# Kernel tuning notes

Hardware: AMD Instinct MI355X
Metric: run time of the kernel (lower is better)

The kernel has to match this reference:

```python
import jax, jax.numpy as jnp
import numpy as np

NUM_HEADS = 12


def setup_inputs() -> dict:
    key = jax.random.key(0)
    ks = jax.random.split(key, 5)
    B, N, C = 64, 388, 768  # N = 8*8*2 + 16*16 + 4
    return {
        "x": jax.random.normal(ks[0], (B, N, C), dtype=jnp.float32),
        "qkv_w": jax.random.normal(ks[1], (3 * C, C), dtype=jnp.float32) * 0.02,
        "qkv_b": jax.random.normal(ks[2], (3 * C,), dtype=jnp.float32) * 0.02,
        "proj_w": jax.random.normal(ks[3], (C, C), dtype=jnp.float32) * 0.02,
        "proj_b": jax.random.normal(ks[4], (C,), dtype=jnp.float32) * 0.02,
        "t_h": 8, "t_w": 8, "s_h": 16, "s_w": 16,
    }


def reference(x, qkv_w, qkv_b, proj_w, proj_b, t_h, t_w, s_h, s_w):
    B, N, C = x.shape
    H = NUM_HEADS
    D = C // H
    scale = D ** -0.5
    L_t = t_h * t_w * 2          # template (x2) tokens
    L_s = s_h * s_w + 4          # search tokens + 4 extra

    qkv = x @ qkv_w.T + qkv_b                       # [B,N,3C]
    qkv = qkv.reshape(B, N, 3, H, D).transpose(2, 0, 3, 1, 4)  # [3,B,H,N,D]
    q, k, v = qkv[0], qkv[1], qkv[2]                # each [B,H,N,D]

    q_mt, q_s = q[:, :, :L_t], q[:, :, L_t:]
    k_mt = k[:, :, :L_t]
    v_mt = v[:, :, :L_t]

    # template self-attention (template queries attend only to template keys)
    attn_mt = jax.nn.softmax(jnp.einsum("bhqd,bhkd->bhqk", q_mt, k_mt) * scale, axis=-1)
    x_mt = jnp.einsum("bhqk,bhkd->bhqd", attn_mt, v_mt)  # [B,H,L_t,D]
    x_mt = x_mt.transpose(0, 2, 1, 3).reshape(B, L_t, C)

    # search queries attend to ALL keys
    attn_s = jax.nn.softmax(jnp.einsum("bhqd,bhkd->bhqk", q_s, k) * scale, axis=-1)
    x_s = jnp.einsum("bhqk,bhkd->bhqd", attn_s, v)  # [B,H,L_s,D]
    x_s = x_s.transpose(0, 2, 1, 3).reshape(B, L_s, C)

    out = jnp.concatenate([x_mt, x_s], axis=1)      # [B,N,C]
    out = out @ proj_w.T + proj_b
    return out
```

## Files before the change

### kernel.cpp

```cpp
#include <hip/hip_runtime.h>
#include <cstdint>
#include <cstddef>
#include <cmath>

typedef __attribute__((ext_vector_type(4))) float f32x4;
typedef __attribute__((ext_vector_type(8))) short bf16x8;

typedef const __attribute__((address_space(1))) void* gas_ptr;
typedef __attribute__((address_space(3))) void* las_ptr;

static __device__ __forceinline__ short f2bf(float f) {
    union { float f; uint32_t u; } v; v.f = f;
    uint32_t r = v.u + 0x7fffu + ((v.u >> 16) & 1u);
    return (short)(r >> 16);
}

constexpr int MP = 25088;

__global__ void cvt_f32_bf16(const float* __restrict__ src, short* __restrict__ dst, int n4) {
    int i = blockIdx.x * blockDim.x + threadIdx.x;
    const int stride = gridDim.x * blockDim.x;
    for (; i < n4; i += stride) {
        const float4 v = reinterpret_cast<const float4*>(src)[i];
        short4 o;
        o.x = f2bf(v.x); o.y = f2bf(v.y); o.z = f2bf(v.z); o.w = f2bf(v.w);
        reinterpret_cast<short4*>(dst)[i] = o;
    }
}

__global__ void cvt_x_pad(const float* __restrict__ src, short* __restrict__ dst) {
    constexpr int N4 = MP * 768 / 4;
    int i = blockIdx.x * blockDim.x + threadIdx.x;
    const int stride = gridDim.x * blockDim.x;
    for (; i < N4; i += stride) {
        const int flat = i * 4;
        const int mp  = flat / 768;
        const int col = flat - mp * 768;
        const int b   = mp / 392;
        const int nn  = mp - b * 392;
        short4 o;
        if (nn < 388) {
            const float4 v = *reinterpret_cast<const float4*>(
                src + ((size_t)(b * 388 + nn) * 768 + col));
            o.x = f2bf(v.x); o.y = f2bf(v.y); o.z = f2bf(v.z); o.w = f2bf(v.w);
        } else {
            o.x = 0; o.y = 0; o.z = 0; o.w = 0;
        }
        reinterpret_cast<short4*>(dst)[i] = o;
    }
}

template<int MODE>
__global__ __launch_bounds__(256) void gemm_bt(
    const short* __restrict__ A, const short* __restrict__ Bw,
    const float* __restrict__ bias,
    short* __restrict__ qk, short* __restrict__ vT,
    float* __restrict__ fo, int NB)
{
    constexpr int K = 768;
    constexpr int KT = 12;
    __shared__ __align__(16) short ldsraw[2 * 128 * 64 * 2];
    short* ldsA = ldsraw;
    short* ldsB = ldsraw + 2 * 128 * 64;

    const int tid  = threadIdx.x;
    const int lane = tid & 63;
    const int wid  = tid >> 6;
    const int lrow = lane & 15;
    const int lgrp = lane >> 4;
    const int wr   = wid >> 1;
    const int wc   = wid & 1;

    const int nwg = gridDim.x;
    const int q8  = nwg >> 3, r8 = nwg & 7;
    const int xcd = blockIdx.x & 7, bidx = blockIdx.x >> 3;
    const int wgid = (xcd < r8 ? xcd * (q8 + 1) : r8 * (q8 + 1) + (xcd - r8) * q8) + bidx;

    int m0, n0;
    if constexpr (MODE == 0) {
        constexpr int G = 14, SG = G * 18;
        const int mg = wgid / SG;
        const int r  = wgid - mg * SG;
        const int n  = r / G;
        const int mi = r - n * G;
        m0 = (mg * G + mi) * 128;
        n0 = n * 128;
    } else {
        m0 = (wgid / NB) * 128;
        n0 = (wgid % NB) * 128;
    }

    f32x4 acc[4][4];
    #pragma unroll
    for (int i = 0; i < 4; ++i)
        #pragma unroll
        for (int j = 0; j < 4; ++j)
            acc[i][j] = f32x4{0.f, 0.f, 0.f, 0.f};

    auto stage = [&](int kt, int buf) {
        #pragma unroll
        for (int it = 0; it < 4; ++it) {
            const int c   = it * 256 + wid * 64 + lane;
            const int row = c >> 3;
            const int scb = ((c & 7) * 16) ^ ((row & 7) << 4);
            const short* ga = A  + (size_t)(m0 + row) * K + kt * 64 + (scb >> 1);
            const short* gb = Bw + (size_t)(n0 + row) * K + kt * 64 + (scb >> 1);
            __builtin_amdgcn_global_load_lds((gas_ptr)ga, (las_ptr)((char*)(ldsA + buf * 128 * 64) + c * 16), 16, 0, 0);
            __builtin_amdgcn_global_load_lds((gas_ptr)gb, (las_ptr)((char*)(ldsB + buf * 128 * 64) + c * 16), 16, 0, 0);
        }
    };

    stage(0, 0);

    for (int kt = 0; kt < KT; ++kt) {
        const int cur = kt & 1;
        if (kt + 1 < KT) {
            stage(kt + 1, cur ^ 1);
            asm volatile("s_waitcnt vmcnt(8)" ::: "memory");
        } else {
            asm volatile("s_waitcnt vmcnt(0)" ::: "memory");
        }
        __builtin_amdgcn_s_barrier();
        __builtin_amdgcn_sched_barrier(0);

        #pragma unroll
        for (int ks = 0; ks < 2; ++ks) {
            bf16x8 af[4], bfv[4];
            #pragma unroll
            for (int i = 0; i < 4; ++i) {
                const int r   = wr * 64 + i * 16 + lrow;
                const int byt = r * 128 + ((ks * 64 + lgrp * 16) ^ ((r & 7) << 4));
                af[i] = *reinterpret_cast<const bf16x8*>((const char*)(ldsA + cur * 128 * 64) + byt);
            }
            #pragma unroll
            for (int j = 0; j < 4; ++j) {
                const int r   = wc * 64 + j * 16 + lrow;
                const int byt = r * 128 + ((ks * 64 + lgrp * 16) ^ ((r & 7) << 4));
                bfv[j] = *reinterpret_cast<const bf16x8*>((const char*)(ldsB + cur * 128 * 64) + byt);
            }
            #pragma unroll
            for (int i = 0; i < 4; ++i)
                #pragma unroll
                for (int j = 0; j < 4; ++j)
                    acc[i][j] = __builtin_amdgcn_mfma_f32_16x16x32_bf16(af[i], bfv[j], acc[i][j], 0, 0, 0);
        }

        __builtin_amdgcn_sched_barrier(0);
        __builtin_amdgcn_s_barrier();
    }

    const int mb = m0 + wr * 64;
    const int nb = n0 + wc * 64;
    if constexpr (MODE == 0) {
        if (n0 < 1536) {
            #pragma unroll
            for (int j = 0; j < 4; ++j) {
                const int c  = nb + j * 16 + lrow;
                const float sc = (c < 768) ? 0.18033688011116f : 1.0f;
                const float bv = bias[c];
                #pragma unroll
                for (int i = 0; i < 4; ++i) {
                    #pragma unroll
                    for (int r = 0; r < 4; ++r) {
                        const int m = mb + i * 16 + lgrp * 4 + r;
                        qk[(size_t)m * 1536 + c] = f2bf((acc[i][j][r] + bv) * sc);
                    }
                }
            }
        } else {
            const int h = (nb - 1536) >> 6;
            short* lw = ldsraw + wid * (64 * 80);
            #pragma unroll
            for (int j = 0; j < 4; ++j) {
                const int dloc = j * 16 + lrow;
                const float bv = bias[nb + j * 16 + lrow];
                #pragma unroll
                for (int i = 0; i < 4; ++i)
                    #pragma unroll
                    for (int r = 0; r < 4; ++r)
                        lw[dloc * 80 + i * 16 + lgrp * 4 + r] = f2bf(acc[i][j][r] + bv);
            }
            asm volatile("s_waitcnt lgkmcnt(0)" ::: "memory");
            __builtin_amdgcn_sched_barrier(0);
            #pragma unroll
            for (int w = 0; w < 8; ++w) {
                const int d    = w * 8 + (lane >> 3);
                const int nloc = (lane & 7) * 8;
                const bf16x8 val = *reinterpret_cast<const bf16x8*>(lw + d * 80 + nloc);
                const int mchunk = mb + nloc;
                const int b  = mchunk / 392;
                const int nn = mchunk - b * 392;
                short* dst = vT + ((size_t)(b * 12 + h) * 64 + d) * 392 + nn;
                *reinterpret_cast<bf16x8*>(dst) = val;
            }
        }
    } else {
        #pragma unroll
        for (int i = 0; i < 4; ++i) {
            #pragma unroll
            for (int r = 0; r < 4; ++r) {
                const int m = mb + i * 16 + lgrp * 4 + r;
                #pragma unroll
                for (int j = 0; j < 4; ++j) {
                    const int c = nb + j * 16 + lrow;
                    fo[(size_t)m * 768 + c] = acc[i][j][r] + bias[c];
                }
            }
        }
    }
}

constexpr int PSTRB = 256;

template<int NT, bool VLDS>
static __device__ __forceinline__ void attn_chunk_lds(
    int kbeg, int k_len,
    const short* __restrict__ klds, const short* __restrict__ vlds,
    const short* __restrict__ vglob,
    const bf16x8 (&qf)[2], char* __restrict__ my,
    int lrow, int lgrp,
    float (&rs)[4], f32x4 (&oacc)[4])
{
    f32x4 sacc[NT];
    #pragma unroll
    for (int t = 0; t < NT; ++t) sacc[t] = f32x4{0.f, 0.f, 0.f, 0.f};

    #pragma unroll
    for (int t = 0; t < NT; ++t) {
        const int kl   = t * 16 + lrow;
        const int byt0 = kl * 128 + ((lgrp * 16) ^ ((kl & 7) << 4));
        const int byt1 = kl * 128 + ((64 + lgrp * 16) ^ ((kl & 7) << 4));
        const bf16x8 k0 = *reinterpret_cast<const bf16x8*>((const char*)klds + byt0);
        const bf16x8 k1 = *reinterpret_cast<const bf16x8*>((const char*)klds + byt1);
        sacc[t] = __builtin_amdgcn_mfma_f32_16x16x32_bf16(qf[0], k0, sacc[t], 0, 0, 0);
        sacc[t] = __builtin_amdgcn_mfma_f32_16x16x32_bf16(qf[1], k1, sacc[t], 0, 0, 0);
    }
    #pragma unroll
    for (int t = 0; t < NT; ++t) {
        const bool bad = (kbeg + t * 16 + lrow >= k_len);
        #pragma unroll
        for (int r = 0; r < 4; ++r) {
            const float p = bad ? 0.f : exp2f(sacc[t][r]);
            rs[r] += p;
            const int row = lgrp * 4 + r;
            const int byt = row * PSTRB + ((t * 32 + lrow * 2) ^ ((row & 7) << 4));
            *reinterpret_cast<short*>(my + byt) = f2bf(p);
        }
    }

    #pragma unroll
    for (int ks = 0; ks < NT / 2; ++ks) {
        const bf16x8 pf = *reinterpret_cast<const bf16x8*>(
            my + lrow * PSTRB + ((ks * 64 + lgrp * 16) ^ ((lrow & 7) << 4)));
        #pragma unroll
        for (int dt = 0; dt < 4; ++dt) {
            const int d = dt * 16 + lrow;
            const bf16x8 vf = VLDS
                ? *reinterpret_cast<const bf16x8*>((const char*)vlds + d * 256 + ((ks * 64 + lgrp * 16) ^ ((d & 7) << 4)))
                : *reinterpret_cast<const bf16x8*>(vglob + (size_t)d * 392 + ks * 32 + lgrp * 8);
            oacc[dt] = __builtin_amdgcn_mfma_f32_16x16x32_bf16(pf, vf, oacc[dt], 0, 0, 0);
        }
    }
}

__global__ __launch_bounds__(256, 2) void attn_flash(
    const short* __restrict__ qkb, const short* __restrict__ vT,
    short* __restrict__ ao)
{
    __shared__ __align__(16) short klds[2][128 * 64];
    __shared__ __align__(16) short vlds[2][64 * 128];
    __shared__ __align__(16) char  plds[4][16 * PSTRB];

    const int tid  = threadIdx.x;
    const int lane = tid & 63;
    const int wid  = tid >> 6;
    const int lrow = lane & 15;
    const int lgrp = lane >> 4;

    const int blk = blockIdx.x;
    const int xcd = blk & 7;
    const int i7  = blk >> 3;
    const int bh  = xcd * 96 + i7 / 7;
    const int bx  = i7 % 7;

    int q_start, qend, k_len, nfull;
    bool tail;
    if (bx < 2) { q_start = bx * 64;             qend = 128; k_len = 128; nfull = 1; tail = false; }
    else        { q_start = 128 + (bx - 2) * 64; qend = 388; k_len = 388; nfull = 3; tail = true;  }

    const int q0 = q_start + wid * 16;

    const int b = bh / 12, h = bh - b * 12;
    const short* qbase = qkb + (size_t)b * 392 * 1536 + h * 64;
    const short* kbase = qbase + 768;
    const short* vbase = vT + (size_t)bh * 64 * 392;

    int qrow = q0 + lrow; if (qrow >= qend) qrow = qend - 1;
    bf16x8 qf[2];
    #pragma unroll
    for (int ks = 0; ks < 2; ++ks)
        qf[ks] = *reinterpret_cast<const bf16x8*>(qbase + (size_t)qrow * 1536 + ks * 32 + lgrp * 8);

    float rs[4] = {0.f, 0.f, 0.f, 0.f};
    f32x4 oacc[4];
    #pragma unroll
    for (int dt = 0; dt < 4; ++dt) oacc[dt] = f32x4{0.f, 0.f, 0.f, 0.f};

    char* my = &plds[wid][0];

    auto stage_full = [&](int ch, int buf) {
        const int kbeg = ch * 128;
        #pragma unroll
        for (int it = 0; it < 4; ++it) {
            const int c = it * 256 + tid;
            const int krow = c >> 3;
            const int kscb = ((c & 7) * 16) ^ ((krow & 7) << 4);
            const short* gk = kbase + (size_t)(kbeg + krow) * 1536 + (kscb >> 1);
            __builtin_amdgcn_global_load_lds((gas_ptr)gk, (las_ptr)((char*)&klds[buf][0] + c * 16), 16, 0, 0);
            const int vrow = c >> 4;
            const int vscb = ((c & 15) * 16) ^ ((vrow & 7) << 4);
            const short* gv = vbase + (size_t)vrow * 392 + kbeg + (vscb >> 1);
            __builtin_amdgcn_global_load_lds((gas_ptr)gv, (las_ptr)((char*)&vlds[buf][0] + c * 16), 16, 0, 0);
        }
    };

    stage_full(0, 0);

    for (int ch = 0; ch < nfull; ++ch) {
        const int cur = ch & 1;
        if (ch + 1 < nfull) {
            stage_full(ch + 1, cur ^ 1);
            asm volatile("s_waitcnt vmcnt(8)" ::: "memory");
        } else {
            asm volatile("s_waitcnt vmcnt(0)" ::: "memory");
        }
        __builtin_amdgcn_s_barrier();
        __builtin_amdgcn_sched_barrier(0);

        attn_chunk_lds<8, true>(ch * 128, k_len, &klds[cur][0], &vlds[cur][0],
                                nullptr, qf, my, lrow, lgrp, rs, oacc);

        __builtin_amdgcn_sched_barrier(0);
        __builtin_amdgcn_s_barrier();
    }

    if (tail) {
        {
            const int c = tid;
            const int krow = c >> 3;
            const int kscb = ((c & 7) * 16) ^ ((krow & 7) << 4);
            int g = 384 + krow; if (g > 391) g = 391;
            const short* gk = kbase + (size_t)g * 1536 + (kscb >> 1);
            __builtin_amdgcn_global_load_lds((gas_ptr)gk, (las_ptr)((char*)&klds[0][0] + c * 16), 16, 0, 0);
        }
        asm volatile("s_waitcnt vmcnt(0)" ::: "memory");
        __builtin_amdgcn_s_barrier();
        __builtin_amdgcn_sched_barrier(0);

        attn_chunk_lds<2, false>(384, k_len, &klds[0][0], nullptr, vbase + 384,
                                 qf, my, lrow, lgrp, rs, oacc);
    }

    #pragma unroll
    for (int msk = 1; msk < 16; msk <<= 1)
        #pragma unroll
        for (int r = 0; r < 4; ++r) rs[r] += __shfl_xor(rs[r], msk, 64);

    float inv[4];
    #pragma unroll
    for (int r = 0; r < 4; ++r) inv[r] = 1.0f / rs[r];
    #pragma unroll
    for (int r = 0; r < 4; ++r) {
        const int qn = q0 + lgrp * 4 + r;
        if (qn < qend) {
            #pragma unroll
            for (int dt = 0; dt < 4; ++dt)
                ao[((size_t)b * 388 + qn) * 768 + h * 64 + dt * 16 + lrow] =
                    f2bf(oacc[dt][r] * inv[r]);
        }
    }
}

extern "C" void kernel_launch(void* const* d_in, const int* in_sizes, int n_in,
                              void* d_out, int out_size, void* d_ws, size_t ws_size,
                              hipStream_t stream) {
    (void)in_sizes; (void)n_in; (void)out_size; (void)ws_size;
    const float* x      = (const float*)d_in[0];
    const float* qkv_w  = (const float*)d_in[1];
    const float* qkv_b  = (const float*)d_in[2];
    const float* proj_w = (const float*)d_in[3];
    const float* proj_b = (const float*)d_in[4];
    float* out = (float*)d_out;

    char* ws = (char*)d_ws;
    short* xb   = (short*)(ws);
    short* attn = (short*)(ws);
    short* qkb  = (short*)(ws + 38535168);
    short* vTb  = (short*)(ws + 115605504);
    short* qwb  = (short*)(ws + 154140672);
    short* pwb  = (short*)(ws + 157679616);

    cvt_x_pad  <<<2048, 256, 0, stream>>>(x, xb);
    cvt_f32_bf16<<<512,  256, 0, stream>>>(qkv_w,  qwb, 2304 * 768 / 4);
    cvt_f32_bf16<<<256,  256, 0, stream>>>(proj_w, pwb, 768 * 768 / 4);

    gemm_bt<0><<<dim3(196 * 18), 256, 0, stream>>>(xb, qwb, qkv_b, qkb, vTb, nullptr, 18);

    attn_flash<<<dim3(5376), 256, 0, stream>>>(qkb, vTb, attn);

    gemm_bt<1><<<dim3(194 * 6), 256, 0, stream>>>(attn, pwb, proj_b, nullptr, nullptr, out, 6);
}
```

Measured before the change: 242.5 us.

## Use 256x256-tile 8-wave phased pipeline for the QKV GEMM

Replaces the templated 128x128 QKV GEMM with a dedicated kernel. It uses 256x256 output tiles, 512 threads (8 waves, each owning 128x64) and a double-buffered 128KB LDS. Each k-step is split into four phases that interleave LDS fragment reads, half-tile async global-to-LDS prefetches and MFMA batches raised with s_setprio. The aim is more operand reuse per loaded byte and better overlap of loads with matrix math. In exchange there are many more barriers, heavy register pressure from 32 accumulators, and only one workgroup per CU because of the LDS footprint. The projection GEMM is split out into its own non-templated kernel with unchanged behavior.

```diff
diff --git a/kernel.cpp b/kernel.cpp
--- a/kernel.cpp
+++ b/kernel.cpp
@@ -50,12 +50,217 @@
     }
 }
 
-template<int MODE>
-__global__ __launch_bounds__(256) void gemm_bt(
+__global__ __launch_bounds__(512, 2) void gemm_qkv_8ph(
     const short* __restrict__ A, const short* __restrict__ Bw,
     const float* __restrict__ bias,
-    short* __restrict__ qk, short* __restrict__ vT,
-    float* __restrict__ fo, int NB)
+    short* __restrict__ qk, short* __restrict__ vT)
+{
+    constexpr int K = 768;
+    constexpr int KT = 12;
+    __shared__ __align__(16) short lds[2][2][256 * 64];
+
+    const int tid  = threadIdx.x;
+    const int lane = tid & 63;
+    const int wid  = tid >> 6;
+    const int lrow = lane & 15;
+    const int lgrp = lane >> 4;
+    const int wr   = wid >> 2;
+    const int wc   = wid & 3;
+
+    const int nwg = gridDim.x;
+    const int q8  = nwg >> 3, r8 = nwg & 7;
+    const int xcd = blockIdx.x & 7, bidx = blockIdx.x >> 3;
+    const int wgid = (xcd < r8 ? xcd * (q8 + 1) : r8 * (q8 + 1) + (xcd - r8) * q8) + bidx;
+    constexpr int G = 14, SG = G * 9;
+    const int mg  = wgid / SG;
+    const int rr_ = wgid - mg * SG;
+    const int nn_ = rr_ / G;
+    const int mi  = rr_ - nn_ * G;
+    const int m0  = (mg * G + mi) * 256;
+    const int n0  = nn_ * 256;
+
+    f32x4 acc[8][4];
+    #pragma unroll
+    for (int i = 0; i < 8; ++i)
+        #pragma unroll
+        for (int j = 0; j < 4; ++j)
+            acc[i][j] = f32x4{0.f, 0.f, 0.f, 0.f};
+
+    auto stage_half = [&](int kt, int buf, int op, int half) {
+        const short* srcp = (op == 0) ? A : Bw;
+        const int rb = (op == 0) ? m0 : n0;
+        #pragma unroll
+        for (int it = 0; it < 2; ++it) {
+            const int c   = half * 1024 + it * 512 + tid;
+            const int row = c >> 3;
+            const int scb = ((c & 7) * 16) ^ ((row & 7) << 4);
+            const short* g = srcp + (size_t)(rb + row) * K + kt * 64 + (scb >> 1);
+            __builtin_amdgcn_global_load_lds((gas_ptr)g,
+                (las_ptr)((char*)&lds[buf][op][0] + c * 16), 16, 0, 0);
+        }
+    };
+
+    auto rdA = [&](int buf, int i, int ks) -> bf16x8 {
+        const int r   = wr * 128 + i * 16 + lrow;
+        const int byt = r * 128 + ((ks * 64 + lgrp * 16) ^ ((r & 7) << 4));
+        return *reinterpret_cast<const bf16x8*>((const char*)&lds[buf][0][0] + byt);
+    };
+    auto rdB = [&](int buf, int j, int ks) -> bf16x8 {
+        const int r   = wc * 64 + j * 16 + lrow;
+        const int byt = r * 128 + ((ks * 64 + lgrp * 16) ^ ((r & 7) << 4));
+        return *reinterpret_cast<const bf16x8*>((const char*)&lds[buf][1][0] + byt);
+    };
+
+    stage_half(0, 0, 0, 0); stage_half(0, 0, 0, 1);
+    stage_half(0, 0, 1, 0); stage_half(0, 0, 1, 1);
+    asm volatile("s_waitcnt vmcnt(0)" ::: "memory");
+    __builtin_amdgcn_s_barrier();
+
+    for (int t = 0; t < KT; ++t) {
+        const int cur = t & 1;
+        const int nxt = cur ^ 1;
+        const bool more = (t + 1 < KT);
+        bf16x8 a03[2][4], a47[2][4], b01[2][2], b23[2][2];
+
+        #pragma unroll
+        for (int ks = 0; ks < 2; ++ks) {
+            #pragma unroll
+            for (int i = 0; i < 4; ++i) a03[ks][i] = rdA(cur, i, ks);
+            #pragma unroll
+            for (int j = 0; j < 2; ++j) b01[ks][j] = rdB(cur, j, ks);
+        }
+        if (more) stage_half(t + 1, nxt, 0, 0);
+        __builtin_amdgcn_s_barrier();
+        asm volatile("s_waitcnt lgkmcnt(0)" ::: "memory");
+        __builtin_amdgcn_sched_barrier(0);
+        __builtin_amdgcn_s_setprio(1);
+        #pragma unroll
+        for (int ks = 0; ks < 2; ++ks)
+            #pragma unroll
+            for (int i = 0; i < 4; ++i)
+                #pragma unroll
+                for (int j = 0; j < 2; ++j)
+                    acc[i][j] = __builtin_amdgcn_mfma_f32_16x16x32_bf16(a03[ks][i], b01[ks][j], acc[i][j], 0, 0, 0);
+        __builtin_amdgcn_s_setprio(0);
+        __builtin_amdgcn_s_barrier();
+
+        #pragma unroll
+        for (int ks = 0; ks < 2; ++ks)
+            #pragma unroll
+            for (int j = 0; j < 2; ++j) b23[ks][j] = rdB(cur, 2 + j, ks);
+        if (more) stage_half(t + 1, nxt, 0, 1);
+        __builtin_amdgcn_s_barrier();
+        asm volatile("s_waitcnt lgkmcnt(0)" ::: "memory");
+        __builtin_amdgcn_sched_barrier(0);
+        __builtin_amdgcn_s_setprio(1);
+        #pragma unroll
+        for (int ks = 0; ks < 2; ++ks)
+            #pragma unroll
+            for (int i = 0; i < 4; ++i)
+                #pragma unroll
+                for (int j = 0; j < 2; ++j)
+                    acc[i][2 + j] = __builtin_amdgcn_mfma_f32_16x16x32_bf16(a03[ks][i], b23[ks][j], acc[i][2 + j], 0, 0, 0);
+        __builtin_amdgcn_s_setprio(0);
+        __builtin_amdgcn_s_barrier();
+
+        #pragma unroll
+        for (int ks = 0; ks < 2; ++ks)
+            #pragma unroll
+            for (int i = 0; i < 4; ++i) a47[ks][i] = rdA(cur, 4 + i, ks);
+        if (more) stage_half(t + 1, nxt, 1, 0);
+        __builtin_amdgcn_s_barrier();
+        asm volatile("s_waitcnt lgkmcnt(0)" ::: "memory");
+        __builtin_amdgcn_sched_barrier(0);
+        __builtin_amdgcn_s_setprio(1);
+        #pragma unroll
+        for (int ks = 0; ks < 2; ++ks)
+            #pragma unroll
+            for (int i = 0; i < 4; ++i)
+                #pragma unroll
+                for (int j = 0; j < 2; ++j)
+                    acc[4 + i][2 + j] = __builtin_amdgcn_mfma_f32_16x16x32_bf16(a47[ks][i], b23[ks][j], acc[4 + i][2 + j], 0, 0, 0);
+        __builtin_amdgcn_s_setprio(0);
+        __builtin_amdgcn_s_barrier();
+
+        #pragma unroll
+        for (int ks = 0; ks < 2; ++ks)
+            #pragma unroll
+            for (int j = 0; j < 2; ++j) b01[ks][j] = rdB(cur, j, ks);
+        if (more) stage_half(t + 1, nxt, 1, 1);
+        __builtin_amdgcn_s_barrier();
+        asm volatile("s_waitcnt lgkmcnt(0)" ::: "memory");
+        __builtin_amdgcn_sched_barrier(0);
+        __builtin_amdgcn_s_setprio(1);
+        #pragma unroll
+        for (int ks = 0; ks < 2; ++ks)
+            #pragma unroll
+            for (int i = 0; i < 4; ++i)
+                #pragma unroll
+                for (int j = 0; j < 2; ++j)
+                    acc[4 + i][j] = __builtin_amdgcn_mfma_f32_16x16x32_bf16(a47[ks][i], b01[ks][j], acc[4 + i][j], 0, 0, 0);
+        __builtin_amdgcn_s_setprio(0);
+
+        __builtin_amdgcn_sched_barrier(0);
+        asm volatile("s_waitcnt vmcnt(0)" ::: "memory");
+        __builtin_amdgcn_s_barrier();
+    }
+
+    const int mb = m0 + wr * 128;
+    const int nb = n0 + wc * 64;
+    if (n0 < 1536) {
+        #pragma unroll
+        for (int j = 0; j < 4; ++j) {
+            const int c  = nb + j * 16 + lrow;
+            const float sc = (c < 768) ? 0.18033688011116f : 1.0f;
+            const float bv = bias[c];
+            #pragma unroll
+            for (int i = 0; i < 8; ++i) {
+                #pragma unroll
+                for (int r = 0; r < 4; ++r) {
+                    const int m = mb + i * 16 + lgrp * 4 + r;
+                    qk[(size_t)m * 1536 + c] = f2bf((acc[i][j][r] + bv) * sc);
+                }
+            }
+        }
+    } else {
+        const int h = (nb - 1536) >> 6;
+        short* lw = (short*)&lds[0][0][0] + wid * (64 * 80);
+        #pragma unroll
+        for (int pass = 0; pass < 2; ++pass) {
+            if (pass) {
+                asm volatile("s_waitcnt lgkmcnt(0)" ::: "memory");
+                __builtin_amdgcn_sched_barrier(0);
+            }
+            #pragma unroll
+            for (int j = 0; j < 4; ++j) {
+                const int dloc = j * 16 + lrow;
+                const float bv = bias[nb + j * 16 + lrow];
+                #pragma unroll
+                for (int ii = 0; ii < 4; ++ii)
+                    #pragma unroll
+                    for (int r = 0; r < 4; ++r)
+                        lw[dloc * 80 + ii * 16 + lgrp * 4 + r] = f2bf(acc[pass * 4 + ii][j][r] + bv);
+            }
+            asm volatile("s_waitcnt lgkmcnt(0)" ::: "memory");
+            __builtin_amdgcn_sched_barrier(0);
+            #pragma unroll
+            for (int w = 0; w < 8; ++w) {
+                const int d    = w * 8 + (lane >> 3);
+                const int nloc = (lane & 7) * 8;
+                const bf16x8 val = *reinterpret_cast<const bf16x8*>(lw + d * 80 + nloc);
+                const int mchunk = mb + pass * 64 + nloc;
+                const int b  = mchunk / 392;
+                const int nn = mchunk - b * 392;
+                short* dst = vT + ((size_t)(b * 12 + h) * 64 + d) * 392 + nn;
+                *reinterpret_cast<bf16x8*>(dst) = val;
+            }
+        }
+    }
+}
+
+__global__ __launch_bounds__(256) void gemm_proj(
+    const short* __restrict__ A, const short* __restrict__ Bw,
+    const float* __restrict__ bias, float* __restrict__ fo, int NB)
 {
     constexpr int K = 768;
     constexpr int KT = 12;
@@ -75,20 +280,8 @@
     const int q8  = nwg >> 3, r8 = nwg & 7;
     const int xcd = blockIdx.x & 7, bidx = blockIdx.x >> 3;
     const int wgid = (xcd < r8 ? xcd * (q8 + 1) : r8 * (q8 + 1) + (xcd - r8) * q8) + bidx;
-
-    int m0, n0;
-    if constexpr (MODE == 0) {
-        constexpr int G = 14, SG = G * 18;
-        const int mg = wgid / SG;
-        const int r  = wgid - mg * SG;
-        const int n  = r / G;
-        const int mi = r - n * G;
-        m0 = (mg * G + mi) * 128;
-        n0 = n * 128;
-    } else {
-        m0 = (wgid / NB) * 128;
-        n0 = (wgid % NB) * 128;
-    }
+    const int m0 = (wgid / NB) * 128;
+    const int n0 = (wgid % NB) * 128;
 
     f32x4 acc[4][4];
     #pragma unroll
@@ -151,60 +344,15 @@
 
     const int mb = m0 + wr * 64;
     const int nb = n0 + wc * 64;
-    if constexpr (MODE == 0) {
-        if (n0 < 1536) {
+    #pragma unroll
+    for (int i = 0; i < 4; ++i) {
+        #pragma unroll
+        for (int r = 0; r < 4; ++r) {
+            const int m = mb + i * 16 + lgrp * 4 + r;
             #pragma unroll
             for (int j = 0; j < 4; ++j) {
-                const int c  = nb + j * 16 + lrow;
-                const float sc = (c < 768) ? 0.18033688011116f : 1.0f;
-                const float bv = bias[c];
-                #pragma unroll
-                for (int i = 0; i < 4; ++i) {
-                    #pragma unroll
-                    for (int r = 0; r < 4; ++r) {
-                        const int m = mb + i * 16 + lgrp * 4 + r;
-                        qk[(size_t)m * 1536 + c] = f2bf((acc[i][j][r] + bv) * sc);
-                    }
-                }
-            }
-        } else {
-            const int h = (nb - 1536) >> 6;
-            short* lw = ldsraw + wid * (64 * 80);
-            #pragma unroll
-            for (int j = 0; j < 4; ++j) {
-                const int dloc = j * 16 + lrow;
-                const float bv = bias[nb + j * 16 + lrow];
-                #pragma unroll
-                for (int i = 0; i < 4; ++i)
-                    #pragma unroll
-                    for (int r = 0; r < 4; ++r)
-                        lw[dloc * 80 + i * 16 + lgrp * 4 + r] = f2bf(acc[i][j][r] + bv);
-            }
-            asm volatile("s_waitcnt lgkmcnt(0)" ::: "memory");
-            __builtin_amdgcn_sched_barrier(0);
-            #pragma unroll
-            for (int w = 0; w < 8; ++w) {
-                const int d    = w * 8 + (lane >> 3);
-                const int nloc = (lane & 7) * 8;
-                const bf16x8 val = *reinterpret_cast<const bf16x8*>(lw + d * 80 + nloc);
-                const int mchunk = mb + nloc;
-                const int b  = mchunk / 392;
-                const int nn = mchunk - b * 392;
-                short* dst = vT + ((size_t)(b * 12 + h) * 64 + d) * 392 + nn;
-                *reinterpret_cast<bf16x8*>(dst) = val;
-            }
-        }
-    } else {
-        #pragma unroll
-        for (int i = 0; i < 4; ++i) {
-            #pragma unroll
-            for (int r = 0; r < 4; ++r) {
-                const int m = mb + i * 16 + lgrp * 4 + r;
-                #pragma unroll
-                for (int j = 0; j < 4; ++j) {
-                    const int c = nb + j * 16 + lrow;
-                    fo[(size_t)m * 768 + c] = acc[i][j][r] + bias[c];
-                }
+                const int c = nb + j * 16 + lrow;
+                fo[(size_t)m * 768 + c] = acc[i][j][r] + bias[c];
             }
         }
     }
@@ -404,9 +552,9 @@
     cvt_f32_bf16<<<512,  256, 0, stream>>>(qkv_w,  qwb, 2304 * 768 / 4);
     cvt_f32_bf16<<<256,  256, 0, stream>>>(proj_w, pwb, 768 * 768 / 4);
 
-    gemm_bt<0><<<dim3(196 * 18), 256, 0, stream>>>(xb, qwb, qkv_b, qkb, vTb, nullptr, 18);
+    gemm_qkv_8ph<<<dim3(98 * 9), 512, 0, stream>>>(xb, qwb, qkv_b, qkb, vTb);
 
     attn_flash<<<dim3(5376), 256, 0, stream>>>(qkb, vTb, attn);
 
-    gemm_bt<1><<<dim3(194 * 6), 256, 0, stream>>>(attn, pwb, proj_b, nullptr, nullptr, out, 6);
-}
+    gemm_proj<<<dim3(194 * 6), 256, 0, stream>>>(attn, pwb, proj_b, out, 6);
+}
```

Result: slower. 272.1 us (+12.2%).

## Replace 128x128 GEMM with 256x256 eight-wave tile and phased prefetch schedule

Applied to the files above, without the earlier changes.

The QKV and projection GEMMs now use 256x256 output tiles with 512 threads, 8 waves and a 128 KB double-buffered LDS. This replaces the 128x128 tiles with 4 waves. The K loop is split into phases that interleave quarter-tile global-to-LDS prefetches with MFMA blocks, using barriers and s_setprio to overlap loads with compute and raise operand reuse. The V-transpose epilogue runs in two passes to fit the larger accumulator. In exchange, fewer and larger workgroups raise register pressure, allow only one block per CU, and may give worse wave-quantization tails.

```diff
diff --git a/kernel.cpp b/kernel.cpp
--- a/kernel.cpp
+++ b/kernel.cpp
@@ -50,26 +50,45 @@
     }
 }
 
+#define PH_SYNC() \
+    __builtin_amdgcn_s_barrier(); \
+    asm volatile("s_waitcnt lgkmcnt(0)" ::: "memory"); \
+    __builtin_amdgcn_sched_barrier(0); \
+    __builtin_amdgcn_s_setprio(1)
+
+#define PH_END() \
+    __builtin_amdgcn_s_setprio(0); \
+    __builtin_amdgcn_s_barrier()
+
+#define MFMA4x2(IOFF, JOFF, B) \
+    _Pragma("unroll") \
+    for (int ks = 0; ks < 2; ++ks) \
+        _Pragma("unroll") \
+        for (int i = 0; i < 4; ++i) \
+            _Pragma("unroll") \
+            for (int j = 0; j < 2; ++j) \
+                acc[(IOFF)+i][(JOFF)+j] = __builtin_amdgcn_mfma_f32_16x16x32_bf16( \
+                    a[ks][i], B[ks][j], acc[(IOFF)+i][(JOFF)+j], 0, 0, 0)
+
 template<int MODE>
-__global__ __launch_bounds__(256) void gemm_bt(
+__global__ __launch_bounds__(512, 2) void gemm256(
     const short* __restrict__ A, const short* __restrict__ Bw,
     const float* __restrict__ bias,
     short* __restrict__ qk, short* __restrict__ vT,
-    float* __restrict__ fo, int NB)
+    float* __restrict__ fo)
 {
     constexpr int K = 768;
     constexpr int KT = 12;
-    __shared__ __align__(16) short ldsraw[2 * 128 * 64 * 2];
-    short* ldsA = ldsraw;
-    short* ldsB = ldsraw + 2 * 128 * 64;
+    constexpr int NU = 6;
+    __shared__ __align__(16) short lds[2][2][256 * 64];
 
     const int tid  = threadIdx.x;
     const int lane = tid & 63;
     const int wid  = tid >> 6;
     const int lrow = lane & 15;
     const int lgrp = lane >> 4;
-    const int wr   = wid >> 1;
-    const int wc   = wid & 1;
+    const int wr   = wid >> 2;
+    const int wc   = wid & 3;
 
     const int nwg = gridDim.x;
     const int q8  = nwg >> 3, r8 = nwg & 7;
@@ -78,78 +97,144 @@
 
     int m0, n0;
     if constexpr (MODE == 0) {
-        constexpr int G = 14, SG = G * 18;
-        const int mg = wgid / SG;
-        const int r  = wgid - mg * SG;
-        const int n  = r / G;
-        const int mi = r - n * G;
-        m0 = (mg * G + mi) * 128;
-        n0 = n * 128;
+        constexpr int G = 14, SG = G * 9;
+        const int mg  = wgid / SG;
+        const int r_  = wgid - mg * SG;
+        const int nn_ = r_ / G;
+        m0 = (mg * G + (r_ - nn_ * G)) * 256;
+        n0 = nn_ * 256;
     } else {
-        m0 = (wgid / NB) * 128;
-        n0 = (wgid % NB) * 128;
-    }
-
-    f32x4 acc[4][4];
-    #pragma unroll
-    for (int i = 0; i < 4; ++i)
+        m0 = (wgid / 3) * 256;
+        n0 = (wgid % 3) * 256;
+    }
+
+    f32x4 acc[8][4];
+    #pragma unroll
+    for (int i = 0; i < 8; ++i)
         #pragma unroll
         for (int j = 0; j < 4; ++j)
             acc[i][j] = f32x4{0.f, 0.f, 0.f, 0.f};
 
-    auto stage = [&](int kt, int buf) {
-        #pragma unroll
-        for (int it = 0; it < 4; ++it) {
-            const int c   = it * 256 + wid * 64 + lane;
+    auto stage_piece = [&](int kt, int buf, int piece) {
+        const int op = (piece == 0 || piece == 3) ? 0 : 1;
+        const short* srcp = op ? Bw : A;
+        const int rb = op ? n0 : m0;
+        #pragma unroll
+        for (int it = 0; it < 2; ++it) {
+            int c;
+            if (piece == 0)      c = it * 1024 + tid;
+            else if (piece == 3) c = it * 1024 + 512 + tid;
+            else {
+                const int idx = it * 512 + tid;
+                const int grp = idx >> 8, win = idx & 255;
+                c = grp * 512 + ((piece == 2) ? 256 : 0) + win;
+            }
             const int row = c >> 3;
             const int scb = ((c & 7) * 16) ^ ((row & 7) << 4);
-            const short* ga = A  + (size_t)(m0 + row) * K + kt * 64 + (scb >> 1);
-            const short* gb = Bw + (size_t)(n0 + row) * K + kt * 64 + (scb >> 1);
-            __builtin_amdgcn_global_load_lds((gas_ptr)ga, (las_ptr)((char*)(ldsA + buf * 128 * 64) + c * 16), 16, 0, 0);
-            __builtin_amdgcn_global_load_lds((gas_ptr)gb, (las_ptr)((char*)(ldsB + buf * 128 * 64) + c * 16), 16, 0, 0);
+            const short* g = srcp + (size_t)(rb + row) * K + kt * 64 + (scb >> 1);
+            __builtin_amdgcn_global_load_lds((gas_ptr)g,
+                (las_ptr)((char*)&lds[buf][op][0] + c * 16), 16, 0, 0);
         }
     };
 
-    stage(0, 0);
-
-    for (int kt = 0; kt < KT; ++kt) {
-        const int cur = kt & 1;
-        if (kt + 1 < KT) {
-            stage(kt + 1, cur ^ 1);
-            asm volatile("s_waitcnt vmcnt(8)" ::: "memory");
-        } else {
-            asm volatile("s_waitcnt vmcnt(0)" ::: "memory");
-        }
+    auto rdA = [&](int buf, int i, int ks) -> bf16x8 {
+        const int r   = wr * 128 + i * 16 + lrow;
+        const int byt = r * 128 + ((ks * 64 + lgrp * 16) ^ ((r & 7) << 4));
+        return *reinterpret_cast<const bf16x8*>((const char*)&lds[buf][0][0] + byt);
+    };
+    auto rdB = [&](int buf, int j, int ks) -> bf16x8 {
+        const int r   = wc * 64 + j * 16 + lrow;
+        const int byt = r * 128 + ((ks * 64 + lgrp * 16) ^ ((r & 7) << 4));
+        return *reinterpret_cast<const bf16x8*>((const char*)&lds[buf][1][0] + byt);
+    };
+
+    stage_piece(0, 0, 0); stage_piece(0, 0, 1); stage_piece(0, 0, 2); stage_piece(0, 0, 3);
+    stage_piece(1, 1, 0); stage_piece(1, 1, 2);
+    asm volatile("s_waitcnt vmcnt(0)" ::: "memory");
+    __builtin_amdgcn_s_barrier();
+
+    bf16x8 a[2][4], bf0[2][2], bf1[2][2];
+
+    for (int u = 0; u < NU; ++u) {
+        const int t1  = 2 * u + 1;
+        const int tn0 = 2 * u + 2;
+        const int tn1 = 2 * u + 3;
+        const bool lastu = (u + 1 == NU);
+
+        #pragma unroll
+        for (int ks = 0; ks < 2; ++ks) {
+            #pragma unroll
+            for (int i = 0; i < 4; ++i) a[ks][i] = rdA(0, i, ks);
+            #pragma unroll
+            for (int j = 0; j < 2; ++j) bf0[ks][j] = rdB(0, j, ks);
+        }
+        stage_piece(t1, 1, 3);
+        PH_SYNC(); MFMA4x2(0, 0, bf0); PH_END();
+
+        #pragma unroll
+        for (int ks = 0; ks < 2; ++ks)
+            #pragma unroll
+            for (int j = 0; j < 2; ++j) bf1[ks][j] = rdB(0, 2 + j, ks);
+        stage_piece(t1, 1, 1);
+        PH_SYNC(); MFMA4x2(0, 2, bf1); PH_END();
+
+        #pragma unroll
+        for (int ks = 0; ks < 2; ++ks)
+            #pragma unroll
+            for (int i = 0; i < 4; ++i) a[ks][i] = rdA(0, 4 + i, ks);
+        if (tn0 < KT) stage_piece(tn0, 0, 0);
+        PH_SYNC(); MFMA4x2(4, 2, bf1); PH_END();
+
+        #pragma unroll
+        for (int ks = 0; ks < 2; ++ks)
+            #pragma unroll
+            for (int j = 0; j < 2; ++j) bf0[ks][j] = rdB(0, j, ks);
+        if (tn0 < KT) stage_piece(tn0, 0, 2);
+        PH_SYNC(); MFMA4x2(4, 0, bf0);
+        __builtin_amdgcn_s_setprio(0);
+        __builtin_amdgcn_sched_barrier(0);
+        if (!lastu) asm volatile("s_waitcnt vmcnt(4)" ::: "memory");
+        else        asm volatile("s_waitcnt vmcnt(0)" ::: "memory");
         __builtin_amdgcn_s_barrier();
+
+        #pragma unroll
+        for (int ks = 0; ks < 2; ++ks) {
+            #pragma unroll
+            for (int i = 0; i < 4; ++i) a[ks][i] = rdA(1, i, ks);
+            #pragma unroll
+            for (int j = 0; j < 2; ++j) bf0[ks][j] = rdB(1, j, ks);
+        }
+        if (tn0 < KT) stage_piece(tn0, 0, 3);
+        PH_SYNC(); MFMA4x2(0, 0, bf0); PH_END();
+
+        #pragma unroll
+        for (int ks = 0; ks < 2; ++ks)
+            #pragma unroll
+            for (int j = 0; j < 2; ++j) bf1[ks][j] = rdB(1, 2 + j, ks);
+        if (tn0 < KT) stage_piece(tn0, 0, 1);
+        PH_SYNC(); MFMA4x2(0, 2, bf1); PH_END();
+
+        #pragma unroll
+        for (int ks = 0; ks < 2; ++ks)
+            #pragma unroll
+            for (int i = 0; i < 4; ++i) a[ks][i] = rdA(1, 4 + i, ks);
+        if (tn1 < KT) stage_piece(tn1, 1, 0);
+        PH_SYNC(); MFMA4x2(4, 2, bf1); PH_END();
+
+        #pragma unroll
+        for (int ks = 0; ks < 2; ++ks)
+            #pragma unroll
+            for (int j = 0; j < 2; ++j) bf0[ks][j] = rdB(1, j, ks);
+        if (tn1 < KT) stage_piece(tn1, 1, 2);
+        PH_SYNC(); MFMA4x2(4, 0, bf0);
+        __builtin_amdgcn_s_setprio(0);
         __builtin_amdgcn_sched_barrier(0);
-
-        #pragma unroll
-        for (int ks = 0; ks < 2; ++ks) {
-            bf16x8 af[4], bfv[4];
-            #pragma unroll
-            for (int i = 0; i < 4; ++i) {
-                const int r   = wr * 64 + i * 16 + lrow;
-                const int byt = r * 128 + ((ks * 64 + lgrp * 16) ^ ((r & 7) << 4));
-                af[i] = *reinterpret_cast<const bf16x8*>((const char*)(ldsA + cur * 128 * 64) + byt);
-            }
-            #pragma unroll
-            for (int j = 0; j < 4; ++j) {
-                const int r   = wc * 64 + j * 16 + lrow;
-                const int byt = r * 128 + ((ks * 64 + lgrp * 16) ^ ((r & 7) << 4));
-                bfv[j] = *reinterpret_cast<const bf16x8*>((const char*)(ldsB + cur * 128 * 64) + byt);
-            }
-            #pragma unroll
-            for (int i = 0; i < 4; ++i)
-                #pragma unroll
-                for (int j = 0; j < 4; ++j)
-                    acc[i][j] = __builtin_amdgcn_mfma_f32_16x16x32_bf16(af[i], bfv[j], acc[i][j], 0, 0, 0);
-        }
-
-        __builtin_amdgcn_sched_barrier(0);
+        if (!lastu) asm volatile("s_waitcnt vmcnt(4)" ::: "memory");
+        else        asm volatile("s_waitcnt vmcnt(0)" ::: "memory");
         __builtin_amdgcn_s_barrier();
     }
 
-    const int mb = m0 + wr * 64;
+    const int mb = m0 + wr * 128;
     const int nb = n0 + wc * 64;
     if constexpr (MODE == 0) {
         if (n0 < 1536) {
@@ -159,7 +244,7 @@
                 const float sc = (c < 768) ? 0.18033688011116f : 1.0f;
                 const float bv = bias[c];
                 #pragma unroll
-                for (int i = 0; i < 4; ++i) {
+                for (int i = 0; i < 8; ++i) {
                     #pragma unroll
                     for (int r = 0; r < 4; ++r) {
                         const int m = mb + i * 16 + lgrp * 4 + r;
@@ -169,34 +254,41 @@
             }
         } else {
             const int h = (nb - 1536) >> 6;
-            short* lw = ldsraw + wid * (64 * 80);
-            #pragma unroll
-            for (int j = 0; j < 4; ++j) {
-                const int dloc = j * 16 + lrow;
-                const float bv = bias[nb + j * 16 + lrow];
+            short* lw = (short*)&lds[0][0][0] + wid * (64 * 80);
+            #pragma unroll
+            for (int pass = 0; pass < 2; ++pass) {
+                if (pass) {
+                    asm volatile("s_waitcnt lgkmcnt(0)" ::: "memory");
+                    __builtin_amdgcn_sched_barrier(0);
+                }
                 #pragma unroll
-                for (int i = 0; i < 4; ++i)
+                for (int j = 0; j < 4; ++j) {
+                    const int dloc = j * 16 + lrow;
+                    const float bv = bias[nb + j * 16 + lrow];
                     #pragma unroll
-                    for (int r = 0; r < 4; ++r)
-                        lw[dloc * 80 + i * 16 + lgrp * 4 + r] = f2bf(acc[i][j][r] + bv);
+                    for (int ii = 0; ii < 4; ++ii)
+                        #pragma unroll
+                        for (int r = 0; r < 4; ++r)
+                            lw[dloc * 80 + ii * 16 + lgrp * 4 + r] = f2bf(acc[pass * 4 + ii][j][r] + bv);
+                }
+                asm volatile("s_waitcnt lgkmcnt(0)" ::: "memory");
+                __builtin_amdgcn_sched_barrier(0);
+                #pragma unroll
+                for (int w = 0; w < 8; ++w) {
+                    const int d    = w * 8 + (lane >> 3);
+                    const int nloc = (lane & 7) * 8;
+                    const bf16x8 val = *reinterpret_cast<const bf16x8*>(lw + d * 80 + nloc);
+                    const int mchunk = mb + pass * 64 + nloc;
+                    const int b  = mchunk / 392;
+                    const int nn = mchunk - b * 392;
+                    short* dst = vT + ((size_t)(b * 12 + h) * 64 + d) * 392 + nn;
+                    *reinterpret_cast<bf16x8*>(dst) = val;
+                }
             }
-            asm volatile("s_waitcnt lgkmcnt(0)" ::: "memory");
-            __builtin_amdgcn_sched_barrier(0);
-            #pragma unroll
-            for (int w = 0; w < 8; ++w) {
-                const int d    = w * 8 + (lane >> 3);
-                const int nloc = (lane & 7) * 8;
-                const bf16x8 val = *reinterpret_cast<const bf16x8*>(lw + d * 80 + nloc);
-                const int mchunk = mb + nloc;
-                const int b  = mchunk / 392;
-                const int nn = mchunk - b * 392;
-                short* dst = vT + ((size_t)(b * 12 + h) * 64 + d) * 392 + nn;
-                *reinterpret_cast<bf16x8*>(dst) = val;
-            }
         }
     } else {
         #pragma unroll
-        for (int i = 0; i < 4; ++i) {
+        for (int i = 0; i < 8; ++i) {
             #pragma unroll
             for (int r = 0; r < 4; ++r) {
                 const int m = mb + i * 16 + lgrp * 4 + r;
@@ -404,9 +496,9 @@
     cvt_f32_bf16<<<512,  256, 0, stream>>>(qkv_w,  qwb, 2304 * 768 / 4);
     cvt_f32_bf16<<<256,  256, 0, stream>>>(proj_w, pwb, 768 * 768 / 4);
 
-    gemm_bt<0><<<dim3(196 * 18), 256, 0, stream>>>(xb, qwb, qkv_b, qkb, vTb, nullptr, 18);
+    gemm256<0><<<dim3(98 * 9), 512, 0, stream>>>(xb, qwb, qkv_b, qkb, vTb, nullptr);
 
     attn_flash<<<dim3(5376), 256, 0, stream>>>(qkb, vTb, attn);
 
-    gemm_bt<1><<<dim3(194 * 6), 256, 0, stream>>>(attn, pwb, proj_b, nullptr, nullptr, out, 6);
-}
+    gemm256<1><<<dim3(97 * 3), 512, 0, stream>>>(attn, pwb, proj_b, nullptr, nullptr, out);
+}
```

Measured after the change: 275.3 us. 1.14x slower.
